# Optimization experiments

Hardware: AMD Instinct MI355X
Metric: run time of the kernel (lower is better)

Reference implementation:

```python
import jax, jax.numpy as jnp
import numpy as np

EMBED_DIM = 1024
NUM_HEADS = 16
HEAD_DIM = EMBED_DIM // NUM_HEADS
B, S = 2, 2048


def _xavier(k, shape):
    # xavier_uniform for square [out,in] weight
    limit = float(np.sqrt(6.0 / (shape[0] + shape[1])))
    return jax.random.uniform(k, shape, jnp.float32, -limit, limit)


def setup_inputs() -> dict:
    key = jax.random.key(0)
    ks = jax.random.split(key, 7)
    return {
        "query": jax.random.normal(ks[0], (B, S, EMBED_DIM), jnp.float32),
        "key": jax.random.normal(ks[1], (B, S, EMBED_DIM), jnp.float32),
        "value": jax.random.normal(ks[2], (B, S, EMBED_DIM), jnp.float32),
        "Wq": _xavier(ks[3], (EMBED_DIM, EMBED_DIM)),
        "Wk": _xavier(ks[4], (EMBED_DIM, EMBED_DIM)),
        "Wv": _xavier(ks[5], (EMBED_DIM, EMBED_DIM)),
        "Wo": _xavier(ks[6], (EMBED_DIM, EMBED_DIM)),
    }


def _orthogonalize(Wq, Wk):
    # Both projections computed from the ORIGINAL weights, then both replaced
    # (matches torch: weight1_proj/weight2_proj computed before copy_).
    Wq_o = Wq - Wq @ (Wk.T @ Wk)
    Wk_o = Wk - Wk @ (Wq.T @ Wq)
    return Wq_o, Wk_o


def reference(query, key, value, Wq, Wk, Wv, Wo):
    Wq_o, Wk_o = _orthogonalize(Wq, Wk)
    # F.linear(x, W) = x @ W.T
    q = query @ Wq_o.T
    k = key @ Wk_o.T
    v = value @ Wv.T
    # [B, S, E] -> [B, H, S, Dh]
    def split_heads(x):
        return x.reshape(B, -1, NUM_HEADS, HEAD_DIM).transpose(0, 2, 1, 3)
    q, k, v = split_heads(q), split_heads(k), split_heads(v)
    scale = 1.0 / (HEAD_DIM ** 0.5)
    scores = jnp.einsum("bhqd,bhkd->bhqk", q, k) * scale
    attn = jax.nn.softmax(scores, axis=-1)
    out = jnp.einsum("bhqk,bhkd->bhqd", attn, v)
    out = out.transpose(0, 2, 1, 3).reshape(B, -1, EMBED_DIM)
    return out @ Wo.T
```

## Files before the change

### kernel.cpp

```cpp
#include <hip/hip_runtime.h>
#include <math.h>

constexpr int EMBED  = 1024;
constexpr int NHEADS = 16;
constexpr int HDIM   = 64;
constexpr int BATCH  = 2;
constexpr int SEQ    = 2048;
constexpr int MROWS  = BATCH * SEQ;

typedef unsigned short u16b;
typedef __attribute__((ext_vector_type(8))) short bfrag;
typedef __attribute__((ext_vector_type(4))) float ffrag;

#define SCALE_Q 0.18033688f

__device__ __forceinline__ u16b f2b(float f) {
    union { float f; unsigned u; } v; v.f = f;
    unsigned r = v.u + 0x7fffu + ((v.u >> 16) & 1u);
    return (u16b)(r >> 16);
}
__device__ __forceinline__ u16b f2b_fast(float f) {
    union { float f; unsigned u; } v; v.f = f;
    return (u16b)((v.u + 0x8000u) >> 16);
}

__device__ __forceinline__ void gload_lds16(const u16b* g, u16b* l) {
    __builtin_amdgcn_global_load_lds(
        (const __attribute__((address_space(1))) void*)g,
        (__attribute__((address_space(3))) void*)l,
        16, 0, 0);
}

struct GemmPtrs {
    const u16b* A[3];
    const u16b* B[3];
    const float* D[3];
    u16b* Cb[3];
    float* Cf[3];
    float scale[3];
    int vt[3];
    int hs[3];
};

__global__ void prep_all(const float* __restrict__ q, const float* __restrict__ k,
                         const float* __restrict__ v,
                         const float* __restrict__ Wq, const float* __restrict__ Wk,
                         const float* __restrict__ Wv, const float* __restrict__ Wo,
                         u16b* __restrict__ oq, u16b* __restrict__ ok, u16b* __restrict__ ov,
                         u16b* __restrict__ wq, u16b* __restrict__ wk,
                         u16b* __restrict__ wv, u16b* __restrict__ wo,
                         u16b* __restrict__ wqt, u16b* __restrict__ wkt) {
    const int z = blockIdx.z;
    const int tid = threadIdx.x;
    if (z < 3) {
        const float* src = (z == 0) ? q : (z == 1) ? k : v;
        u16b* dst = (z == 0) ? oq : (z == 1) ? ok : ov;
        const int i = blockIdx.x * 256 + tid;
        float4 val = ((const float4*)src)[i];
        ushort4 o;
        o.x = f2b(val.x); o.y = f2b(val.y); o.z = f2b(val.z); o.w = f2b(val.w);
        ((ushort4*)dst)[i] = o;
        return;
    }
    if (blockIdx.x >= 1024) return;
    const int w = z - 3;
    const float* src = (w == 0) ? Wq : (w == 1) ? Wk : (w == 2) ? Wv : Wo;
    u16b* dst  = (w == 0) ? wq : (w == 1) ? wk : (w == 2) ? wv : wo;
    u16b* dstT = (w == 0) ? wqt : (w == 1) ? wkt : nullptr;
    __shared__ float t[32][33];
    const int bx = (blockIdx.x & 31) * 32, by = (blockIdx.x >> 5) * 32;
    const int x = tid & 31, y = tid >> 5;
#pragma unroll
    for (int r = 0; r < 4; ++r) {
        const int row = by + y + 8 * r;
        const float val = src[(size_t)row * EMBED + bx + x];
        dst[(size_t)row * EMBED + bx + x] = f2b(val);
        if (w < 2) t[y + 8 * r][x] = val;
    }
    if (w >= 2) return;
    __syncthreads();
#pragma unroll
    for (int r = 0; r < 4; ++r)
        dstT[(size_t)(bx + y + 8 * r) * EMBED + by + x] = f2b(t[x][y + 8 * r]);
}

template<int MODE>
__global__ __launch_bounds__(256) void gemm64(GemmPtrs p, int M, int N, int K) {
    const int z = blockIdx.z;
    const u16b* __restrict__ A = p.A[z];
    const u16b* __restrict__ B = p.B[z];
    const float* __restrict__ D = p.D[z];
    u16b* __restrict__ Cb = p.Cb[z];
    const float scale = p.scale[z];

    __shared__ __align__(16) u16b As[64 * 32];
    __shared__ __align__(16) u16b Bs[64 * 32];

    const int tid = threadIdx.x;
    const int wave = tid >> 6, lane = tid & 63;
    const int quad = lane >> 4, l16 = lane & 15;
    const int wrow = wave >> 1, wcol = wave & 1;
    const int m0 = blockIdx.y * 64, n0 = blockIdx.x * 64;

    ffrag acc[2][2];
#pragma unroll
    for (int i = 0; i < 2; ++i)
#pragma unroll
        for (int j = 0; j < 2; ++j) acc[i][j] = ffrag{0.f, 0.f, 0.f, 0.f};

    const int srow = tid >> 2, schunk = tid & 3;

    for (int kt = 0; kt < K; kt += 32) {
        gload_lds16(A + (size_t)(m0 + srow) * K + kt + schunk * 8, &As[wave * 512]);
        gload_lds16(B + (size_t)(n0 + srow) * K + kt + schunk * 8, &Bs[wave * 512]);
        __syncthreads();
        bfrag a[2], bv[2];
#pragma unroll
        for (int i = 0; i < 2; ++i)
            a[i] = *(const bfrag*)&As[(wrow * 32 + i * 16 + l16) * 32 + quad * 8];
#pragma unroll
        for (int j = 0; j < 2; ++j)
            bv[j] = *(const bfrag*)&Bs[(wcol * 32 + j * 16 + l16) * 32 + quad * 8];
#pragma unroll
        for (int i = 0; i < 2; ++i)
#pragma unroll
            for (int j = 0; j < 2; ++j)
                acc[i][j] = __builtin_amdgcn_mfma_f32_16x16x32_bf16(a[i], bv[j], acc[i][j], 0, 0, 0);
        __syncthreads();
    }

#pragma unroll
    for (int i = 0; i < 2; ++i)
#pragma unroll
        for (int j = 0; j < 2; ++j) {
            const int col = n0 + wcol * 32 + j * 16 + l16;
#pragma unroll
            for (int r = 0; r < 4; ++r) {
                const int row = m0 + wrow * 32 + i * 16 + quad * 4 + r;
                const size_t idx = (size_t)row * N + col;
                const float v = acc[i][j][r];
                if (MODE == 0) Cb[idx] = f2b(v * scale);
                else Cb[idx] = f2b(D[idx] - v);
            }
        }
}

template<int MODE>
__global__ __launch_bounds__(256) void gemm128(GemmPtrs p, int M, int N, int K) {
    const int z = blockIdx.z;
    const u16b* __restrict__ A = p.A[z];
    const u16b* __restrict__ B = p.B[z];
    u16b* __restrict__ Cb = p.Cb[z];
    float* __restrict__ Cf = p.Cf[z];
    const float scale = p.scale[z];
    const int vt = p.vt[z], hs = p.hs[z];

    constexpr int BK = 32;
    __shared__ __align__(16) u16b As[128 * BK];
    __shared__ __align__(16) u16b Bs[128 * BK];

    const int tid = threadIdx.x;
    const int wave = tid >> 6, lane = tid & 63;
    const int quad = lane >> 4, l16 = lane & 15;
    const int wrow = wave >> 1, wcol = wave & 1;
    const int m0 = blockIdx.y * 128, n0 = blockIdx.x * 128;

    ffrag acc[4][4];
#pragma unroll
    for (int i = 0; i < 4; ++i)
#pragma unroll
        for (int j = 0; j < 4; ++j) acc[i][j] = ffrag{0.f, 0.f, 0.f, 0.f};

    const int srow = lane >> 2, schunk = lane & 3;

    for (int kt = 0; kt < K; kt += BK) {
#pragma unroll
        for (int q = 0; q < 2; ++q) {
            int row = wave * 32 + q * 16;
            gload_lds16(A + (size_t)(m0 + row + srow) * K + kt + schunk * 8, &As[row * BK]);
            gload_lds16(B + (size_t)(n0 + row + srow) * K + kt + schunk * 8, &Bs[row * BK]);
        }
        __syncthreads();
        bfrag af[4], bfv[4];
#pragma unroll
        for (int i = 0; i < 4; ++i)
            af[i] = *(const bfrag*)&As[(wrow * 64 + i * 16 + l16) * BK + quad * 8];
#pragma unroll
        for (int j = 0; j < 4; ++j)
            bfv[j] = *(const bfrag*)&Bs[(wcol * 64 + j * 16 + l16) * BK + quad * 8];
#pragma unroll
        for (int i = 0; i < 4; ++i)
#pragma unroll
            for (int j = 0; j < 4; ++j)
                acc[i][j] = __builtin_amdgcn_mfma_f32_16x16x32_bf16(af[i], bfv[j], acc[i][j], 0, 0, 0);
        __syncthreads();
    }

    if (MODE == 0 && vt) {
#pragma unroll
        for (int i = 0; i < 4; ++i)
#pragma unroll
            for (int j = 0; j < 4; ++j) {
                const int col = n0 + wcol * 64 + j * 16 + l16;
                const int h = col >> 6, d = col & 63;
                const int row0 = m0 + wrow * 64 + i * 16 + quad * 4;
                const int b = row0 >> 11, s = row0 & 2047;
                ushort4 o;
                o.x = f2b(acc[i][j][0]); o.y = f2b(acc[i][j][1]);
                o.z = f2b(acc[i][j][2]); o.w = f2b(acc[i][j][3]);
                *(ushort4*)&Cb[((size_t)(b * NHEADS + h) * HDIM + d) * SEQ + s] = o;
            }
        return;
    }
    if (MODE == 0 && hs) {
#pragma unroll
        for (int i = 0; i < 4; ++i)
#pragma unroll
            for (int j = 0; j < 4; ++j) {
                const int col = n0 + wcol * 64 + j * 16 + l16;
                const int h = col >> 6, d = col & 63;
                const int row0 = m0 + wrow * 64 + i * 16 + quad * 4;
                const int b = row0 >> 11, s0 = row0 & 2047;
#pragma unroll
                for (int r = 0; r < 4; ++r)
                    Cb[((size_t)(b * NHEADS + h) * SEQ + s0 + r) * HDIM + d] =
                        f2b(acc[i][j][r] * scale);
            }
        return;
    }

#pragma unroll
    for (int i = 0; i < 4; ++i)
#pragma unroll
        for (int j = 0; j < 4; ++j) {
            const int col = n0 + wcol * 64 + j * 16 + l16;
#pragma unroll
            for (int r = 0; r < 4; ++r) {
                const int row = m0 + wrow * 64 + i * 16 + quad * 4 + r;
                const size_t idx = (size_t)row * N + col;
                const float v = acc[i][j][r];
                if (MODE == 0) Cb[idx] = f2b(v * scale);
                else Cf[idx] = v;
            }
        }
}

__global__ __launch_bounds__(256) void flash_attn4(
    const u16b* __restrict__ Qp, const u16b* __restrict__ Kp,
    const u16b* __restrict__ Vt, u16b* __restrict__ Oo)
{
    const int tid = threadIdx.x;
    const int wave = tid >> 6, lane = tid & 63;
    const int quad = lane >> 4, l16 = lane & 15;
    const int qt = blockIdx.x, h = blockIdx.y, b = blockIdx.z;
    const int qb = qt * 128 + wave * 32;

    __shared__ __align__(16) u16b Ks[2][64 * 64];
    __shared__ __align__(16) u16b Vs[2][64 * 64];
    __shared__ __align__(16) u16b Ps[4][2][16][72];

    const size_t hsbase = (size_t)(b * NHEADS + h) * SEQ;
    const size_t vtbase = (size_t)(b * NHEADS + h) * HDIM * SEQ;
    const size_t obase  = (size_t)b * SEQ * EMBED + h * HDIM;

    bfrag bq[2][2];
#pragma unroll
    for (int u = 0; u < 2; ++u)
#pragma unroll
        for (int s = 0; s < 2; ++s)
            bq[u][s] = *(const bfrag*)&Qp[(hsbase + qb + u * 16 + l16) * HDIM + s * 32 + quad * 8];

    ffrag ov[2][4];
#pragma unroll
    for (int u = 0; u < 2; ++u)
#pragma unroll
        for (int t = 0; t < 4; ++t) ov[u][t] = ffrag{0.f, 0.f, 0.f, 0.f};
    float l_run[2] = {0.f, 0.f};

    const int r0 = tid >> 3, c0 = tid & 7;
    const int sw0 = (r0 * 8 + (c0 ^ (r0 & 7))) * 8;
    const int sw1 = ((r0 + 32) * 8 + (c0 ^ (r0 & 7))) * 8;
    const u16b* kgb = Kp + hsbase * HDIM;
    const u16b* vgb = Vt + vtbase;

    {
        bfrag k0 = *(const bfrag*)(kgb + tid * 8);
        bfrag k1 = *(const bfrag*)(kgb + (tid + 256) * 8);
        bfrag v0 = *(const bfrag*)(vgb + (size_t)r0 * SEQ + c0 * 8);
        bfrag v1 = *(const bfrag*)(vgb + (size_t)(r0 + 32) * SEQ + c0 * 8);
        *(bfrag*)&Ks[0][sw0] = k0;  *(bfrag*)&Ks[0][sw1] = k1;
        *(bfrag*)&Vs[0][sw0] = v0;  *(bfrag*)&Vs[0][sw1] = v1;
    }
    __syncthreads();

    int p = 0;
    for (int kt = 0; kt < SEQ; kt += 64, p ^= 1) {
        const bool more = (kt + 64) < SEQ;
        bfrag kn0, kn1, vn0, vn1;
        if (more) {
            const u16b* kg = kgb + (size_t)(kt + 64) * HDIM;
            kn0 = *(const bfrag*)(kg + tid * 8);
            kn1 = *(const bfrag*)(kg + (tid + 256) * 8);
            vn0 = *(const bfrag*)(vgb + (size_t)r0 * SEQ + kt + 64 + c0 * 8);
            vn1 = *(const bfrag*)(vgb + (size_t)(r0 + 32) * SEQ + kt + 64 + c0 * 8);
        }

        ffrag St[2][4];
#pragma unroll
        for (int u = 0; u < 2; ++u)
#pragma unroll
            for (int t = 0; t < 4; ++t) St[u][t] = ffrag{0.f, 0.f, 0.f, 0.f};
#pragma unroll
        for (int t = 0; t < 4; ++t) {
            const int row = t * 16 + l16;
#pragma unroll
            for (int s = 0; s < 2; ++s) {
                const int ch = quad + s * 4;
                bfrag kf = *(const bfrag*)&Ks[p][(row * 8 + (ch ^ (row & 7))) * 8];
#pragma unroll
                for (int u = 0; u < 2; ++u)
                    St[u][t] = __builtin_amdgcn_mfma_f32_16x16x32_bf16(kf, bq[u][s], St[u][t], 0, 0, 0);
            }
        }

#pragma unroll
        for (int u = 0; u < 2; ++u) {
            float rs = 0.f;
#pragma unroll
            for (int t = 0; t < 4; ++t)
#pragma unroll
                for (int r = 0; r < 4; ++r) {
                    const float pv = __builtin_amdgcn_exp2f(St[u][t][r]);
                    St[u][t][r] = pv;
                    rs += pv;
                }
            rs += __shfl_xor(rs, 16);
            rs += __shfl_xor(rs, 32);
            l_run[u] += rs;
        }

#pragma unroll
        for (int u = 0; u < 2; ++u)
#pragma unroll
            for (int t = 0; t < 4; ++t) {
                ushort4 pk;
                pk.x = f2b_fast(St[u][t][0]); pk.y = f2b_fast(St[u][t][1]);
                pk.z = f2b_fast(St[u][t][2]); pk.w = f2b_fast(St[u][t][3]);
                *(ushort4*)&Ps[wave][u][l16][t * 16 + quad * 4] = pk;
            }
        asm volatile("s_waitcnt lgkmcnt(0)" ::: "memory");
        bfrag bp[2][2];
#pragma unroll
        for (int u = 0; u < 2; ++u)
#pragma unroll
            for (int s = 0; s < 2; ++s)
                bp[u][s] = *(const bfrag*)&Ps[wave][u][l16][s * 32 + quad * 8];

#pragma unroll
        for (int t = 0; t < 4; ++t) {
            const int row = t * 16 + l16;
#pragma unroll
            for (int s = 0; s < 2; ++s) {
                const int ch = quad + s * 4;
                bfrag vf = *(const bfrag*)&Vs[p][(row * 8 + (ch ^ (row & 7))) * 8];
#pragma unroll
                for (int u = 0; u < 2; ++u)
                    ov[u][t] = __builtin_amdgcn_mfma_f32_16x16x32_bf16(vf, bp[u][s], ov[u][t], 0, 0, 0);
            }
        }

        if (more) {
            *(bfrag*)&Ks[p ^ 1][sw0] = kn0;  *(bfrag*)&Ks[p ^ 1][sw1] = kn1;
            *(bfrag*)&Vs[p ^ 1][sw0] = vn0;  *(bfrag*)&Vs[p ^ 1][sw1] = vn1;
            __syncthreads();
        }
    }

#pragma unroll
    for (int u = 0; u < 2; ++u) {
        const float inv = 1.f / l_run[u];
#pragma unroll
        for (int t = 0; t < 4; ++t) {
            ushort4 o;
            o.x = f2b(ov[u][t][0] * inv); o.y = f2b(ov[u][t][1] * inv);
            o.z = f2b(ov[u][t][2] * inv); o.w = f2b(ov[u][t][3] * inv);
            *(ushort4*)&Oo[obase + (size_t)(qb + u * 16 + l16) * EMBED + t * 16 + quad * 4] = o;
        }
    }
}

extern "C" void kernel_launch(void* const* d_in, const int* in_sizes, int n_in,
                              void* d_out, int out_size, void* d_ws, size_t ws_size,
                              hipStream_t stream) {
    const float* query = (const float*)d_in[0];
    const float* key_  = (const float*)d_in[1];
    const float* value = (const float*)d_in[2];
    const float* Wq    = (const float*)d_in[3];
    const float* Wk    = (const float*)d_in[4];
    const float* Wv    = (const float*)d_in[5];
    const float* Wo    = (const float*)d_in[6];
    float* out = (float*)d_out;

    char* ws = (char*)d_ws;
    const size_t MB = 1024 * 1024;
    u16b* xq  = (u16b*)(ws + 0 * MB);
    u16b* xk  = (u16b*)(ws + 8 * MB);
    u16b* xv  = (u16b*)(ws + 16 * MB);
    u16b* wq  = (u16b*)(ws + 24 * MB);
    u16b* wk  = (u16b*)(ws + 26 * MB);
    u16b* wv  = (u16b*)(ws + 28 * MB);
    u16b* wo  = (u16b*)(ws + 30 * MB);
    u16b* wqt = (u16b*)(ws + 32 * MB);
    u16b* wkt = (u16b*)(ws + 34 * MB);
    u16b* gq  = (u16b*)(ws + 36 * MB);
    u16b* gk  = (u16b*)(ws + 38 * MB);
    u16b* wqo = (u16b*)(ws + 40 * MB);
    u16b* wko = (u16b*)(ws + 42 * MB);
    u16b* qp  = (u16b*)(ws + 44 * MB);
    u16b* kp  = (u16b*)(ws + 52 * MB);
    u16b* Vt  = (u16b*)(ws + 68 * MB);
    u16b* ao  = xq;

    prep_all<<<dim3(MROWS * EMBED / 1024, 1, 7), dim3(256), 0, stream>>>(
        query, key_, value, Wq, Wk, Wv, Wo,
        xq, xk, xv, wq, wk, wv, wo, wqt, wkt);

    {
        GemmPtrs p{};
        p.A[0] = wqt; p.B[0] = wqt; p.Cb[0] = gq; p.scale[0] = 1.f;
        p.A[1] = wkt; p.B[1] = wkt; p.Cb[1] = gk; p.scale[1] = 1.f;
        gemm64<0><<<dim3(16, 16, 2), dim3(256), 0, stream>>>(p, EMBED, EMBED, EMBED);
    }
    {
        GemmPtrs p{};
        p.A[0] = wq; p.B[0] = gk; p.D[0] = Wq; p.Cb[0] = wqo;
        p.A[1] = wk; p.B[1] = gq; p.D[1] = Wk; p.Cb[1] = wko;
        gemm64<1><<<dim3(16, 16, 2), dim3(256), 0, stream>>>(p, EMBED, EMBED, EMBED);
    }
    {
        GemmPtrs p{};
        p.A[0] = xq; p.B[0] = wqo; p.Cb[0] = qp; p.scale[0] = SCALE_Q; p.hs[0] = 1;
        p.A[1] = xk; p.B[1] = wko; p.Cb[1] = kp; p.scale[1] = 1.f;     p.hs[1] = 1;
        p.A[2] = xv; p.B[2] = wv;  p.Cb[2] = Vt; p.scale[2] = 1.f;     p.vt[2] = 1;
        gemm128<0><<<dim3(EMBED / 128, MROWS / 128, 3), dim3(256), 0, stream>>>(
            p, MROWS, EMBED, EMBED);
    }
    flash_attn4<<<dim3(SEQ / 128, NHEADS, BATCH), dim3(256), 0, stream>>>(qp, kp, Vt, ao);
    {
        GemmPtrs p{};
        p.A[0] = ao; p.B[0] = wo; p.Cf[0] = out; p.scale[0] = 1.f;
        gemm128<2><<<dim3(EMBED / 128, MROWS / 128, 1), dim3(256), 0, stream>>>(
            p, MROWS, EMBED, EMBED);
    }
}
```

Before: 296.4 us.

## Split attention KV range in two with a combine pass; shrink output GEMM tile

The flash-attention kernel now splits the key sequence into two halves across separate blocks, which doubles the grid. Each half writes an unnormalized fp32 partial output and its row sums, and a new combine kernel adds the halves, normalizes them and converts to bf16. The GEMM is templated on its M tile so the output projection can use 64-row tiles, doubling that grid for better CU coverage. In exchange, the split adds fp32 partial-output traffic and an extra kernel launch, and the workspace buffers are rearranged so they alias in time.

```diff
diff --git a/kernel.cpp b/kernel.cpp
--- a/kernel.cpp
+++ b/kernel.cpp
@@ -145,8 +145,8 @@
         }
 }
 
-template<int MODE>
-__global__ __launch_bounds__(256) void gemm128(GemmPtrs p, int M, int N, int K) {
+template<int MODE, int BM>
+__global__ __launch_bounds__(256) void gemm_big(GemmPtrs p, int M, int N, int K) {
     const int z = blockIdx.z;
     const u16b* __restrict__ A = p.A[z];
     const u16b* __restrict__ B = p.B[z];
@@ -156,40 +156,46 @@
     const int vt = p.vt[z], hs = p.hs[z];
 
     constexpr int BK = 32;
-    __shared__ __align__(16) u16b As[128 * BK];
+    constexpr int IT = BM / 32;
+    constexpr int IA = BM / 64;
+    __shared__ __align__(16) u16b As[BM * BK];
     __shared__ __align__(16) u16b Bs[128 * BK];
 
     const int tid = threadIdx.x;
     const int wave = tid >> 6, lane = tid & 63;
     const int quad = lane >> 4, l16 = lane & 15;
     const int wrow = wave >> 1, wcol = wave & 1;
-    const int m0 = blockIdx.y * 128, n0 = blockIdx.x * 128;
-
-    ffrag acc[4][4];
-#pragma unroll
-    for (int i = 0; i < 4; ++i)
+    const int m0 = blockIdx.y * BM, n0 = blockIdx.x * 128;
+
+    ffrag acc[IT][4];
+#pragma unroll
+    for (int i = 0; i < IT; ++i)
 #pragma unroll
         for (int j = 0; j < 4; ++j) acc[i][j] = ffrag{0.f, 0.f, 0.f, 0.f};
 
     const int srow = lane >> 2, schunk = lane & 3;
 
     for (int kt = 0; kt < K; kt += BK) {
+#pragma unroll
+        for (int q = 0; q < IA; ++q) {
+            int row = wave * (BM / 4) + q * 16;
+            gload_lds16(A + (size_t)(m0 + row + srow) * K + kt + schunk * 8, &As[row * BK]);
+        }
 #pragma unroll
         for (int q = 0; q < 2; ++q) {
             int row = wave * 32 + q * 16;
-            gload_lds16(A + (size_t)(m0 + row + srow) * K + kt + schunk * 8, &As[row * BK]);
             gload_lds16(B + (size_t)(n0 + row + srow) * K + kt + schunk * 8, &Bs[row * BK]);
         }
         __syncthreads();
-        bfrag af[4], bfv[4];
-#pragma unroll
-        for (int i = 0; i < 4; ++i)
-            af[i] = *(const bfrag*)&As[(wrow * 64 + i * 16 + l16) * BK + quad * 8];
+        bfrag af[IT], bfv[4];
+#pragma unroll
+        for (int i = 0; i < IT; ++i)
+            af[i] = *(const bfrag*)&As[(wrow * (BM / 2) + i * 16 + l16) * BK + quad * 8];
 #pragma unroll
         for (int j = 0; j < 4; ++j)
             bfv[j] = *(const bfrag*)&Bs[(wcol * 64 + j * 16 + l16) * BK + quad * 8];
 #pragma unroll
-        for (int i = 0; i < 4; ++i)
+        for (int i = 0; i < IT; ++i)
 #pragma unroll
             for (int j = 0; j < 4; ++j)
                 acc[i][j] = __builtin_amdgcn_mfma_f32_16x16x32_bf16(af[i], bfv[j], acc[i][j], 0, 0, 0);
@@ -198,12 +204,12 @@
 
     if (MODE == 0 && vt) {
 #pragma unroll
-        for (int i = 0; i < 4; ++i)
+        for (int i = 0; i < IT; ++i)
 #pragma unroll
             for (int j = 0; j < 4; ++j) {
                 const int col = n0 + wcol * 64 + j * 16 + l16;
                 const int h = col >> 6, d = col & 63;
-                const int row0 = m0 + wrow * 64 + i * 16 + quad * 4;
+                const int row0 = m0 + wrow * (BM / 2) + i * 16 + quad * 4;
                 const int b = row0 >> 11, s = row0 & 2047;
                 ushort4 o;
                 o.x = f2b(acc[i][j][0]); o.y = f2b(acc[i][j][1]);
@@ -214,12 +220,12 @@
     }
     if (MODE == 0 && hs) {
 #pragma unroll
-        for (int i = 0; i < 4; ++i)
+        for (int i = 0; i < IT; ++i)
 #pragma unroll
             for (int j = 0; j < 4; ++j) {
                 const int col = n0 + wcol * 64 + j * 16 + l16;
                 const int h = col >> 6, d = col & 63;
-                const int row0 = m0 + wrow * 64 + i * 16 + quad * 4;
+                const int row0 = m0 + wrow * (BM / 2) + i * 16 + quad * 4;
                 const int b = row0 >> 11, s0 = row0 & 2047;
 #pragma unroll
                 for (int r = 0; r < 4; ++r)
@@ -230,13 +236,13 @@
     }
 
 #pragma unroll
-    for (int i = 0; i < 4; ++i)
+    for (int i = 0; i < IT; ++i)
 #pragma unroll
         for (int j = 0; j < 4; ++j) {
             const int col = n0 + wcol * 64 + j * 16 + l16;
 #pragma unroll
             for (int r = 0; r < 4; ++r) {
-                const int row = m0 + wrow * 64 + i * 16 + quad * 4 + r;
+                const int row = m0 + wrow * (BM / 2) + i * 16 + quad * 4 + r;
                 const size_t idx = (size_t)row * N + col;
                 const float v = acc[i][j][r];
                 if (MODE == 0) Cb[idx] = f2b(v * scale);
@@ -245,15 +251,18 @@
         }
 }
 
-__global__ __launch_bounds__(256) void flash_attn4(
+__global__ __launch_bounds__(256) void flash_attn5(
     const u16b* __restrict__ Qp, const u16b* __restrict__ Kp,
-    const u16b* __restrict__ Vt, u16b* __restrict__ Oo)
+    const u16b* __restrict__ Vt, float* __restrict__ Opart,
+    float* __restrict__ Lpart)
 {
     const int tid = threadIdx.x;
     const int wave = tid >> 6, lane = tid & 63;
     const int quad = lane >> 4, l16 = lane & 15;
-    const int qt = blockIdx.x, h = blockIdx.y, b = blockIdx.z;
+    const int qt = blockIdx.x, h = blockIdx.y;
+    const int b = blockIdx.z >> 1, sp = blockIdx.z & 1;
     const int qb = qt * 128 + wave * 32;
+    const int kt0 = sp * (SEQ / 2), kt1 = kt0 + SEQ / 2;
 
     __shared__ __align__(16) u16b Ks[2][64 * 64];
     __shared__ __align__(16) u16b Vs[2][64 * 64];
@@ -261,7 +270,7 @@
 
     const size_t hsbase = (size_t)(b * NHEADS + h) * SEQ;
     const size_t vtbase = (size_t)(b * NHEADS + h) * HDIM * SEQ;
-    const size_t obase  = (size_t)b * SEQ * EMBED + h * HDIM;
+    const size_t obase  = ((size_t)sp * MROWS + (size_t)b * SEQ) * EMBED + h * HDIM;
 
     bfrag bq[2][2];
 #pragma unroll
@@ -284,18 +293,19 @@
     const u16b* vgb = Vt + vtbase;
 
     {
-        bfrag k0 = *(const bfrag*)(kgb + tid * 8);
-        bfrag k1 = *(const bfrag*)(kgb + (tid + 256) * 8);
-        bfrag v0 = *(const bfrag*)(vgb + (size_t)r0 * SEQ + c0 * 8);
-        bfrag v1 = *(const bfrag*)(vgb + (size_t)(r0 + 32) * SEQ + c0 * 8);
+        const u16b* kg = kgb + (size_t)kt0 * HDIM;
+        bfrag k0 = *(const bfrag*)(kg + tid * 8);
+        bfrag k1 = *(const bfrag*)(kg + (tid + 256) * 8);
+        bfrag v0 = *(const bfrag*)(vgb + (size_t)r0 * SEQ + kt0 + c0 * 8);
+        bfrag v1 = *(const bfrag*)(vgb + (size_t)(r0 + 32) * SEQ + kt0 + c0 * 8);
         *(bfrag*)&Ks[0][sw0] = k0;  *(bfrag*)&Ks[0][sw1] = k1;
         *(bfrag*)&Vs[0][sw0] = v0;  *(bfrag*)&Vs[0][sw1] = v1;
     }
     __syncthreads();
 
     int p = 0;
-    for (int kt = 0; kt < SEQ; kt += 64, p ^= 1) {
-        const bool more = (kt + 64) < SEQ;
+    for (int kt = kt0; kt < kt1; kt += 64, p ^= 1) {
+        const bool more = (kt + 64) < kt1;
         bfrag kn0, kn1, vn0, vn1;
         if (more) {
             const u16b* kg = kgb + (size_t)(kt + 64) * HDIM;
@@ -378,15 +388,32 @@
 
 #pragma unroll
     for (int u = 0; u < 2; ++u) {
-        const float inv = 1.f / l_run[u];
 #pragma unroll
         for (int t = 0; t < 4; ++t) {
-            ushort4 o;
-            o.x = f2b(ov[u][t][0] * inv); o.y = f2b(ov[u][t][1] * inv);
-            o.z = f2b(ov[u][t][2] * inv); o.w = f2b(ov[u][t][3] * inv);
-            *(ushort4*)&Oo[obase + (size_t)(qb + u * 16 + l16) * EMBED + t * 16 + quad * 4] = o;
-        }
-    }
+            float4 o;
+            o.x = ov[u][t][0]; o.y = ov[u][t][1];
+            o.z = ov[u][t][2]; o.w = ov[u][t][3];
+            *(float4*)&Opart[obase + (size_t)(qb + u * 16 + l16) * EMBED + t * 16 + quad * 4] = o;
+        }
+        if (quad == 0)
+            Lpart[((size_t)sp * BATCH * NHEADS + b * NHEADS + h) * SEQ + qb + u * 16 + l16] = l_run[u];
+    }
+}
+
+__global__ void combine_o(const float* __restrict__ O0, const float* __restrict__ O1,
+                          const float* __restrict__ L0, const float* __restrict__ L1,
+                          u16b* __restrict__ ao) {
+    const int i = blockIdx.x * 256 + threadIdx.x;
+    const int e0 = i << 2;
+    const int row = e0 >> 10, col = e0 & 1023;
+    const int lidx = ((row >> 11) * NHEADS + (col >> 6)) * SEQ + (row & 2047);
+    float4 a = ((const float4*)O0)[i];
+    float4 c = ((const float4*)O1)[i];
+    const float inv = 1.f / (L0[lidx] + L1[lidx]);
+    ushort4 o;
+    o.x = f2b((a.x + c.x) * inv); o.y = f2b((a.y + c.y) * inv);
+    o.z = f2b((a.z + c.z) * inv); o.w = f2b((a.w + c.w) * inv);
+    ((ushort4*)ao)[i] = o;
 }
 
 extern "C" void kernel_launch(void* const* d_in, const int* in_sizes, int n_in,
@@ -409,17 +436,19 @@
     u16b* wq  = (u16b*)(ws + 24 * MB);
     u16b* wk  = (u16b*)(ws + 26 * MB);
     u16b* wv  = (u16b*)(ws + 28 * MB);
-    u16b* wo  = (u16b*)(ws + 30 * MB);
-    u16b* wqt = (u16b*)(ws + 32 * MB);
-    u16b* wkt = (u16b*)(ws + 34 * MB);
-    u16b* gq  = (u16b*)(ws + 36 * MB);
-    u16b* gk  = (u16b*)(ws + 38 * MB);
-    u16b* wqo = (u16b*)(ws + 40 * MB);
-    u16b* wko = (u16b*)(ws + 42 * MB);
+    u16b* gq  = (u16b*)(ws + 32 * MB);
+    u16b* gk  = (u16b*)(ws + 34 * MB);
+    u16b* wqo = (u16b*)(ws + 36 * MB);
+    u16b* wko = (u16b*)(ws + 38 * MB);
+    u16b* wo  = (u16b*)(ws + 40 * MB);
     u16b* qp  = (u16b*)(ws + 44 * MB);
     u16b* kp  = (u16b*)(ws + 52 * MB);
-    u16b* Vt  = (u16b*)(ws + 68 * MB);
-    u16b* ao  = xq;
+    u16b* Vt  = (u16b*)(ws + 60 * MB);
+    u16b* wqt = (u16b*)(ws + 60 * MB);
+    u16b* wkt = (u16b*)(ws + 62 * MB);
+    float* Op  = (float*)(ws + 0 * MB);
+    float* Lp  = (float*)(ws + 32 * MB);
+    u16b*  ao  = (u16b*)(ws + 44 * MB);
 
     prep_all<<<dim3(MROWS * EMBED / 1024, 1, 7), dim3(256), 0, stream>>>(
         query, key_, value, Wq, Wk, Wv, Wo,
@@ -442,14 +471,17 @@
         p.A[0] = xq; p.B[0] = wqo; p.Cb[0] = qp; p.scale[0] = SCALE_Q; p.hs[0] = 1;
         p.A[1] = xk; p.B[1] = wko; p.Cb[1] = kp; p.scale[1] = 1.f;     p.hs[1] = 1;
         p.A[2] = xv; p.B[2] = wv;  p.Cb[2] = Vt; p.scale[2] = 1.f;     p.vt[2] = 1;
-        gemm128<0><<<dim3(EMBED / 128, MROWS / 128, 3), dim3(256), 0, stream>>>(
+        gemm_big<0, 128><<<dim3(EMBED / 128, MROWS / 128, 3), dim3(256), 0, stream>>>(
             p, MROWS, EMBED, EMBED);
     }
-    flash_attn4<<<dim3(SEQ / 128, NHEADS, BATCH), dim3(256), 0, stream>>>(qp, kp, Vt, ao);
+    flash_attn5<<<dim3(SEQ / 128, NHEADS, BATCH * 2), dim3(256), 0, stream>>>(
+        qp, kp, Vt, Op, Lp);
+    combine_o<<<dim3(MROWS * EMBED / 1024), dim3(256), 0, stream>>>(
+        Op, Op + (size_t)MROWS * EMBED, Lp, Lp + (size_t)BATCH * NHEADS * SEQ, ao);
     {
         GemmPtrs p{};
         p.A[0] = ao; p.B[0] = wo; p.Cf[0] = out; p.scale[0] = 1.f;
-        gemm128<2><<<dim3(EMBED / 128, MROWS / 128, 1), dim3(256), 0, stream>>>(
+        gemm_big<2, 64><<<dim3(EMBED / 128, MROWS / 64, 1), dim3(256), 0, stream>>>(
             p, MROWS, EMBED, EMBED);
     }
 }
```

After: 294.9 us. About the same (-0.5%).
